# Optimization experiments

Measured on AMD Instinct MI355X. Metric: run time of the kernel, lower is better.

## Reference

```python
import jax, jax.numpy as jnp
import numpy as np

H = 50  # hidden size

def setup_inputs() -> dict:
    key = jax.random.key(0)
    k_in, k_wx, k_wh, k_wd = jax.random.split(key, 4)
    B, T, D = 1024, 2048, 1
    inputs = jax.random.normal(k_in, (B, T, D), dtype=jnp.float32)
    # fused gate weights, gate order (i, f, g, o) -> 4H columns
    Wx = jax.random.normal(k_wx, (D, 4 * H), dtype=jnp.float32) * 0.1
    Wh = jax.random.normal(k_wh, (H, 4 * H), dtype=jnp.float32) * 0.1
    b = jnp.zeros((4 * H,), dtype=jnp.float32)
    Wd = jax.random.normal(k_wd, (H, 1), dtype=jnp.float32) * 0.1
    bd = jnp.zeros((1,), dtype=jnp.float32)
    return {"inputs": inputs, "Wx": Wx, "Wh": Wh, "b": b, "Wd": Wd, "bd": bd}

def _lstm_last_hidden(inputs, Wx, Wh, b):
    B = inputs.shape[0]
    c0 = jnp.zeros((B, H), dtype=inputs.dtype)
    h0 = jnp.zeros((B, H), dtype=inputs.dtype)

    def step(carry, x_t):
        c, h = carry
        z = x_t @ Wx + h @ Wh + b          # [B, 4H]
        i, f, g, o = jnp.split(z, 4, axis=-1)
        i = jax.nn.sigmoid(i)
        f = jax.nn.sigmoid(f)
        g = jnp.tanh(g)
        o = jax.nn.sigmoid(o)
        c_new = f * c + i * g
        h_new = o * jnp.tanh(c_new)
        return (c_new, h_new), None

    xs = jnp.swapaxes(inputs, 0, 1)        # [T, B, D] for scan over time
    (c_fin, h_fin), _ = jax.lax.scan(step, (c0, h0), xs)
    return h_fin                            # [B, H]

def reference(inputs, Wx, Wh, b, Wd, bd):
    h_last = _lstm_last_hidden(inputs, Wx, Wh, b)
    return h_last @ Wd + bd                # [B, 1]
```

## Files before the change

kernel.cpp:

```cpp
#include <hip/hip_runtime.h>

#define HID 50
#define FOURH 200
#define TSTEPS 2048
#define NBATCH 1024

#define LOG2E 1.44269504f

typedef _Float16 v2h __attribute__((ext_vector_type(2)));

__device__ __forceinline__ float frcp(float x)  { return __builtin_amdgcn_rcpf(x); }
__device__ __forceinline__ float fexp2(float x) { return __builtin_amdgcn_exp2f(x); }
__device__ __forceinline__ v2h bc_v2h(unsigned int u) {
    return __builtin_bit_cast(v2h, u);
}

__global__ __launch_bounds__(64, 1)
void lstm_trans_kernel(const float* __restrict__ x,
                       const float* __restrict__ Wx,
                       const float* __restrict__ Wh,
                       const float* __restrict__ bias,
                       const float* __restrict__ Wd,
                       const float* __restrict__ bd,
                       float* __restrict__ out) {
    const int b    = blockIdx.x;
    const int lane = threadIdx.x;
    const int lc   = (lane < HID) ? lane : (HID - 1);

    __shared__ __align__(16) float xs[TSTEPS + 8];

    const float4* xb4 = (const float4*)(x + (size_t)b * TSTEPS);
    float4* xs4 = (float4*)xs;
    #pragma unroll
    for (int i = lane; i < TSTEPS / 4; i += 64) xs4[i] = xb4[i];
    if (lane < 8) xs[TSTEPS + lane] = 0.0f;

    const float SNEG = -LOG2E;
    const float S2L  = 2.0f * LOG2E;
    v2h wi[25], wf[25], wg[25], wo[25];
    #pragma unroll
    for (int k2 = 0; k2 < 25; ++k2) {
        const float* r0 = Wh + (2 * k2) * FOURH;
        const float* r1 = Wh + (2 * k2 + 1) * FOURH;
        wi[k2] = v2h{(_Float16)(SNEG * r0[lc]),           (_Float16)(SNEG * r1[lc])};
        wf[k2] = v2h{(_Float16)(SNEG * r0[HID + lc]),     (_Float16)(SNEG * r1[HID + lc])};
        wg[k2] = v2h{(_Float16)(S2L  * r0[2 * HID + lc]), (_Float16)(S2L  * r1[2 * HID + lc])};
        wo[k2] = v2h{(_Float16)(SNEG * r0[3 * HID + lc]), (_Float16)(SNEG * r1[3 * HID + lc])};
    }
    const float wx_i = SNEG * Wx[lc],           b_i = SNEG * bias[lc];
    const float wx_f = SNEG * Wx[HID + lc],     b_f = SNEG * bias[HID + lc];
    const float wx_g = S2L  * Wx[2 * HID + lc], b_g = S2L  * bias[2 * HID + lc];
    const float wx_o = SNEG * Wx[3 * HID + lc], b_o = SNEG * bias[3 * HID + lc];

    float cs = 0.0f;
    float h  = 0.0f;
    __syncthreads();

    const float4* xsv = (const float4*)xs;
    float4 xq = xsv[0];

    for (int tb = 0; tb < TSTEPS; tb += 4) {
        const float4 xq_next = xsv[(tb >> 2) + 1];

        #pragma unroll
        for (int s = 0; s < 4; ++s) {
            const float xt = (s == 0) ? xq.x : (s == 1) ? xq.y
                           : (s == 2) ? xq.z : xq.w;

            const int hi32 = __builtin_bit_cast(int, h);
            const int hn32 = __builtin_amdgcn_update_dpp(
                0, hi32, 0x101 , 0xf, 0xf, true);
            const float hn = __builtin_bit_cast(float, hn32);
            const unsigned hp =
                __builtin_bit_cast(unsigned, __builtin_amdgcn_cvt_pkrtz(h, hn));
            unsigned sh[25];
            #pragma unroll
            for (int k = 0; k < 25; ++k)
                sh[k] = (unsigned)__builtin_amdgcn_readlane((int)hp, 2 * k);

            float zi = fmaf(xt, wx_i, b_i);
            #pragma unroll
            for (int j = 0; j < 25; ++j)
                zi = __builtin_amdgcn_fdot2(wi[j], bc_v2h(sh[j]), zi, false);
            const float ei = fexp2(zi);

            float zg = fmaf(xt, wx_g, b_g);
            #pragma unroll
            for (int j = 0; j < 25; ++j)
                zg = __builtin_amdgcn_fdot2(wg[j], bc_v2h(sh[j]), zg, false);
            const float eg = fexp2(zg);

            const float den1 = (1.0f + ei) * (1.0f + eg);
            const float r1   = frcp(den1);
            const float num1 = fmaf(eg, S2L, -S2L);
            const float prod = num1 * r1;

            float zf = fmaf(xt, wx_f, b_f);
            #pragma unroll
            for (int j = 0; j < 25; ++j)
                zf = __builtin_amdgcn_fdot2(wf[j], bc_v2h(sh[j]), zf, false);
            const float ef = fexp2(zf);
            const float fg = frcp(1.0f + ef);

            const float cs_new = fmaf(fg, cs, prod);
            const float ec = fexp2(cs_new);

            float zo = fmaf(xt, wx_o, b_o);
            #pragma unroll
            for (int j = 0; j < 25; ++j)
                zo = __builtin_amdgcn_fdot2(wo[j], bc_v2h(sh[j]), zo, false);
            const float eo = fexp2(zo);

            const float den2 = (1.0f + eo) * (1.0f + ec);
            const float r2   = frcp(den2);
            const float num2 = ec - 1.0f;
            cs = cs_new;
            h  = num2 * r2;
        }

        xq = xq_next;
    }

    float v = (lane < HID) ? h * Wd[lane] : 0.0f;
    #pragma unroll
    for (int off = 32; off > 0; off >>= 1) v += __shfl_down(v, off);
    if (lane == 0) out[b] = v + bd[0];
}

extern "C" void kernel_launch(void* const* d_in, const int* in_sizes, int n_in,
                              void* d_out, int out_size, void* d_ws, size_t ws_size,
                              hipStream_t stream) {
    const float* x    = (const float*)d_in[0];
    const float* Wx   = (const float*)d_in[1];
    const float* Wh   = (const float*)d_in[2];
    const float* bias = (const float*)d_in[3];
    const float* Wd   = (const float*)d_in[4];
    const float* bd   = (const float*)d_in[5];
    float* out = (float*)d_out;

    lstm_trans_kernel<<<dim3(NBATCH), dim3(64), 0, stream>>>(
        x, Wx, Wh, bias, Wd, bd, out);
}
```

Before: 642.7 us.

## Broadcast half of hidden state via LDS, fuse gate dot loops and reciprocals

Splits the per-step broadcast of the hidden state: the first 24 elements still go through readlane, and the remaining 26 are written as fp16 to a small LDS buffer and read back as vector loads. This cuts the number of scalar readlane instructions on the serial recurrence path. It also interleaves the i/g/f dot-product chains for more instruction-level parallelism and merges the forget-gate reciprocal into a single rcp. The LDS write-then-read within one wave has no explicit barrier and depends on in-order LDS access within the wave. The added LDS round trip sits on the recurrence's critical latency path.

```diff
diff --git a/kernel.cpp b/kernel.cpp
--- a/kernel.cpp
+++ b/kernel.cpp
@@ -16,24 +16,26 @@
 }
 
 __global__ __launch_bounds__(64, 1)
-void lstm_trans_kernel(const float* __restrict__ x,
-                       const float* __restrict__ Wx,
-                       const float* __restrict__ Wh,
-                       const float* __restrict__ bias,
-                       const float* __restrict__ Wd,
-                       const float* __restrict__ bd,
-                       float* __restrict__ out) {
+void lstm_hyb_kernel(const float* __restrict__ x,
+                     const float* __restrict__ Wx,
+                     const float* __restrict__ Wh,
+                     const float* __restrict__ bias,
+                     const float* __restrict__ Wd,
+                     const float* __restrict__ bd,
+                     float* __restrict__ out) {
     const int b    = blockIdx.x;
     const int lane = threadIdx.x;
     const int lc   = (lane < HID) ? lane : (HID - 1);
 
-    __shared__ __align__(16) float xs[TSTEPS + 8];
+    __shared__ __align__(16) float    xs[TSTEPS + 8];
+    __shared__ __align__(16) _Float16 hbuf[80];
 
     const float4* xb4 = (const float4*)(x + (size_t)b * TSTEPS);
     float4* xs4 = (float4*)xs;
     #pragma unroll
     for (int i = lane; i < TSTEPS / 4; i += 64) xs4[i] = xb4[i];
     if (lane < 8) xs[TSTEPS + lane] = 0.0f;
+    for (int i = lane; i < 80; i += 64) hbuf[i] = (_Float16)0.0f;
 
     const float SNEG = -LOG2E;
     const float S2L  = 2.0f * LOG2E;
@@ -52,6 +54,8 @@
     const float wx_g = S2L  * Wx[2 * HID + lc], b_g = S2L  * bias[2 * HID + lc];
     const float wx_o = SNEG * Wx[3 * HID + lc], b_o = SNEG * bias[3 * HID + lc];
 
+    const int widx = (lane < HID) ? lane : (lane + 14);
+
     float cs = 0.0f;
     float h  = 0.0f;
     __syncthreads();
@@ -67,55 +71,76 @@
             const float xt = (s == 0) ? xq.x : (s == 1) ? xq.y
                            : (s == 2) ? xq.z : xq.w;
 
+            const uint4    q0  = *(const uint4*)(hbuf + 24);
+            const uint4    q1  = *(const uint4*)(hbuf + 32);
+            const uint4    q2  = *(const uint4*)(hbuf + 40);
+            const unsigned q3  = *(const unsigned*)(hbuf + 48);
+            const unsigned hl[13] = {q0.x, q0.y, q0.z, q0.w,
+                                     q1.x, q1.y, q1.z, q1.w,
+                                     q2.x, q2.y, q2.z, q2.w, q3};
+
             const int hi32 = __builtin_bit_cast(int, h);
             const int hn32 = __builtin_amdgcn_update_dpp(
                 0, hi32, 0x101 , 0xf, 0xf, true);
             const float hn = __builtin_bit_cast(float, hn32);
             const unsigned hp =
                 __builtin_bit_cast(unsigned, __builtin_amdgcn_cvt_pkrtz(h, hn));
-            unsigned sh[25];
+            unsigned sh[12];
             #pragma unroll
-            for (int k = 0; k < 25; ++k)
+            for (int k = 0; k < 12; ++k)
                 sh[k] = (unsigned)__builtin_amdgcn_readlane((int)hp, 2 * k);
 
             float zi = fmaf(xt, wx_i, b_i);
-            #pragma unroll
-            for (int j = 0; j < 25; ++j)
-                zi = __builtin_amdgcn_fdot2(wi[j], bc_v2h(sh[j]), zi, false);
-            const float ei = fexp2(zi);
-
             float zg = fmaf(xt, wx_g, b_g);
-            #pragma unroll
-            for (int j = 0; j < 25; ++j)
-                zg = __builtin_amdgcn_fdot2(wg[j], bc_v2h(sh[j]), zg, false);
-            const float eg = fexp2(zg);
-
-            const float den1 = (1.0f + ei) * (1.0f + eg);
-            const float r1   = frcp(den1);
-            const float num1 = fmaf(eg, S2L, -S2L);
-            const float prod = num1 * r1;
-
             float zf = fmaf(xt, wx_f, b_f);
             #pragma unroll
-            for (int j = 0; j < 25; ++j)
-                zf = __builtin_amdgcn_fdot2(wf[j], bc_v2h(sh[j]), zf, false);
+            for (int j = 0; j < 12; ++j) {
+                const v2h hj = bc_v2h(sh[j]);
+                zi = __builtin_amdgcn_fdot2(wi[j], hj, zi, false);
+                zg = __builtin_amdgcn_fdot2(wg[j], hj, zg, false);
+                zf = __builtin_amdgcn_fdot2(wf[j], hj, zf, false);
+            }
+            #pragma unroll
+            for (int j = 0; j < 13; ++j) {
+                const v2h hj = bc_v2h(hl[j]);
+                zi = __builtin_amdgcn_fdot2(wi[12 + j], hj, zi, false);
+                zg = __builtin_amdgcn_fdot2(wg[12 + j], hj, zg, false);
+                zf = __builtin_amdgcn_fdot2(wf[12 + j], hj, zf, false);
+            }
+            const float ei = fexp2(zi);
+            const float eg = fexp2(zg);
             const float ef = fexp2(zf);
-            const float fg = frcp(1.0f + ef);
 
-            const float cs_new = fmaf(fg, cs, prod);
+            const float a1   = 1.0f + ei;
+            const float a2   = 1.0f + eg;
+            const float den1 = a1 * a2;
+            const float num1 = fmaf(eg, S2L, -S2L);
+            const float a3   = 1.0f + ef;
+            const float dd   = den1 * a3;
+            const float rr   = frcp(dd);
+            const float m1   = num1 * a3;
+            const float tnum = fmaf(cs, den1, m1);
+            const float cs_new = tnum * rr;
             const float ec = fexp2(cs_new);
 
             float zo = fmaf(xt, wx_o, b_o);
             #pragma unroll
-            for (int j = 0; j < 25; ++j)
+            for (int j = 0; j < 12; ++j)
                 zo = __builtin_amdgcn_fdot2(wo[j], bc_v2h(sh[j]), zo, false);
+            #pragma unroll
+            for (int j = 0; j < 13; ++j)
+                zo = __builtin_amdgcn_fdot2(wo[12 + j], bc_v2h(hl[j]), zo, false);
             const float eo = fexp2(zo);
 
-            const float den2 = (1.0f + eo) * (1.0f + ec);
+            const float a4   = 1.0f + eo;
+            const float a5   = 1.0f + ec;
+            const float den2 = a4 * a5;
             const float r2   = frcp(den2);
             const float num2 = ec - 1.0f;
             cs = cs_new;
             h  = num2 * r2;
+
+            hbuf[widx] = (_Float16)h;
         }
 
         xq = xq_next;
@@ -138,6 +163,6 @@
     const float* bd   = (const float*)d_in[5];
     float* out = (float*)d_out;
 
-    lstm_trans_kernel<<<dim3(NBATCH), dim3(64), 0, stream>>>(
+    lstm_hyb_kernel<<<dim3(NBATCH), dim3(64), 0, stream>>>(
         x, Wx, Wh, bias, Wd, bd, out);
 }
```

Result: no change. 648.2 us (+0.9%).

## Interleave gate dot chains, merge reciprocals, and shorten neighbour-hidden exchange path

Applied to the files above, without the earlier changes.

Runs the i, g and f gate dot-product chains interleaved in one loop so the dependent fdot2 sequences can overlap. The cell update now uses a single reciprocal over the product of the three denominators instead of two. The DPP neighbour shuffle is applied to the numerator and reciprocal as soon as they exist, and hn is rebuilt by a multiply, which moves the exchange off the h-to-readlane critical path. The bias/input affine terms use packed float2 arithmetic. Combining three denominators into one product may lose range or precision.

```diff
diff --git a/kernel.cpp b/kernel.cpp
--- a/kernel.cpp
+++ b/kernel.cpp
@@ -8,6 +8,7 @@
 #define LOG2E 1.44269504f
 
 typedef _Float16 v2h __attribute__((ext_vector_type(2)));
+typedef float    f32x2 __attribute__((ext_vector_type(2)));
 
 __device__ __forceinline__ float frcp(float x)  { return __builtin_amdgcn_rcpf(x); }
 __device__ __forceinline__ float fexp2(float x) { return __builtin_amdgcn_exp2f(x); }
@@ -16,13 +17,13 @@
 }
 
 __global__ __launch_bounds__(64, 1)
-void lstm_trans_kernel(const float* __restrict__ x,
-                       const float* __restrict__ Wx,
-                       const float* __restrict__ Wh,
-                       const float* __restrict__ bias,
-                       const float* __restrict__ Wd,
-                       const float* __restrict__ bd,
-                       float* __restrict__ out) {
+void lstm_pk_kernel(const float* __restrict__ x,
+                    const float* __restrict__ Wx,
+                    const float* __restrict__ Wh,
+                    const float* __restrict__ bias,
+                    const float* __restrict__ Wd,
+                    const float* __restrict__ bd,
+                    float* __restrict__ out) {
     const int b    = blockIdx.x;
     const int lane = threadIdx.x;
     const int lc   = (lane < HID) ? lane : (HID - 1);
@@ -47,13 +48,14 @@
         wg[k2] = v2h{(_Float16)(S2L  * r0[2 * HID + lc]), (_Float16)(S2L  * r1[2 * HID + lc])};
         wo[k2] = v2h{(_Float16)(SNEG * r0[3 * HID + lc]), (_Float16)(SNEG * r1[3 * HID + lc])};
     }
-    const float wx_i = SNEG * Wx[lc],           b_i = SNEG * bias[lc];
-    const float wx_f = SNEG * Wx[HID + lc],     b_f = SNEG * bias[HID + lc];
-    const float wx_g = S2L  * Wx[2 * HID + lc], b_g = S2L  * bias[2 * HID + lc];
-    const float wx_o = SNEG * Wx[3 * HID + lc], b_o = SNEG * bias[3 * HID + lc];
+    const f32x2 wx_if = {SNEG * Wx[lc],           SNEG * Wx[HID + lc]};
+    const f32x2 b_if  = {SNEG * bias[lc],         SNEG * bias[HID + lc]};
+    const f32x2 wx_go = {S2L  * Wx[2 * HID + lc], SNEG * Wx[3 * HID + lc]};
+    const f32x2 b_go  = {S2L  * bias[2 * HID + lc], SNEG * bias[3 * HID + lc]};
 
     float cs = 0.0f;
     float h  = 0.0f;
+    float hn = 0.0f;
     __syncthreads();
 
     const float4* xsv = (const float4*)xs;
@@ -67,10 +69,6 @@
             const float xt = (s == 0) ? xq.x : (s == 1) ? xq.y
                            : (s == 2) ? xq.z : xq.w;
 
-            const int hi32 = __builtin_bit_cast(int, h);
-            const int hn32 = __builtin_amdgcn_update_dpp(
-                0, hi32, 0x101 , 0xf, 0xf, true);
-            const float hn = __builtin_bit_cast(float, hn32);
             const unsigned hp =
                 __builtin_bit_cast(unsigned, __builtin_amdgcn_cvt_pkrtz(h, hn));
             unsigned sh[25];
@@ -78,44 +76,53 @@
             for (int k = 0; k < 25; ++k)
                 sh[k] = (unsigned)__builtin_amdgcn_readlane((int)hp, 2 * k);
 
-            float zi = fmaf(xt, wx_i, b_i);
+            const f32x2 xt2 = {xt, xt};
+            const f32x2 zif0 = xt2 * wx_if + b_if;
+            const f32x2 zgo0 = xt2 * wx_go + b_go;
+            float zi = zif0.x, zf = zif0.y, zg = zgo0.x, zo = zgo0.y;
+
+            #pragma unroll
+            for (int j = 0; j < 25; ++j) {
+                const v2h hj = bc_v2h(sh[j]);
+                zi = __builtin_amdgcn_fdot2(wi[j], hj, zi, false);
+                zg = __builtin_amdgcn_fdot2(wg[j], hj, zg, false);
+                zf = __builtin_amdgcn_fdot2(wf[j], hj, zf, false);
+            }
+            const float ei = fexp2(zi);
+            const float eg = fexp2(zg);
+            const float ef = fexp2(zf);
+
+            const f32x2 eig = {ei, eg};
+            const f32x2 a12 = eig + f32x2{1.0f, 1.0f};
+            const float den1 = a12.x * a12.y;
+            const float num1 = fmaf(eg, S2L, -S2L);
+            const float a3   = 1.0f + ef;
+            const float dd   = den1 * a3;
+            const float rr   = frcp(dd);
+            const float m1   = num1 * a3;
+            const float tnum = fmaf(cs, den1, m1);
+            const float cs_new = tnum * rr;
+            const float ec = fexp2(cs_new);
+
+            float zov = zo;
             #pragma unroll
             for (int j = 0; j < 25; ++j)
-                zi = __builtin_amdgcn_fdot2(wi[j], bc_v2h(sh[j]), zi, false);
-            const float ei = fexp2(zi);
+                zov = __builtin_amdgcn_fdot2(wo[j], bc_v2h(sh[j]), zov, false);
+            const float eo = fexp2(zov);
 
-            float zg = fmaf(xt, wx_g, b_g);
-            #pragma unroll
-            for (int j = 0; j < 25; ++j)
-                zg = __builtin_amdgcn_fdot2(wg[j], bc_v2h(sh[j]), zg, false);
-            const float eg = fexp2(zg);
-
-            const float den1 = (1.0f + ei) * (1.0f + eg);
-            const float r1   = frcp(den1);
-            const float num1 = fmaf(eg, S2L, -S2L);
-            const float prod = num1 * r1;
-
-            float zf = fmaf(xt, wx_f, b_f);
-            #pragma unroll
-            for (int j = 0; j < 25; ++j)
-                zf = __builtin_amdgcn_fdot2(wf[j], bc_v2h(sh[j]), zf, false);
-            const float ef = fexp2(zf);
-            const float fg = frcp(1.0f + ef);
-
-            const float cs_new = fmaf(fg, cs, prod);
-            const float ec = fexp2(cs_new);
-
-            float zo = fmaf(xt, wx_o, b_o);
-            #pragma unroll
-            for (int j = 0; j < 25; ++j)
-                zo = __builtin_amdgcn_fdot2(wo[j], bc_v2h(sh[j]), zo, false);
-            const float eo = fexp2(zo);
-
-            const float den2 = (1.0f + eo) * (1.0f + ec);
+            const f32x2 eoc = {eo, ec};
+            const f32x2 a45 = eoc + f32x2{1.0f, 1.0f};
+            const float den2 = a45.x * a45.y;
             const float r2   = frcp(den2);
             const float num2 = ec - 1.0f;
             cs = cs_new;
             h  = num2 * r2;
+
+            const int n2 = __builtin_amdgcn_update_dpp(
+                0, __builtin_bit_cast(int, num2), 0x101, 0xf, 0xf, true);
+            const int r2n = __builtin_amdgcn_update_dpp(
+                0, __builtin_bit_cast(int, r2), 0x101, 0xf, 0xf, true);
+            hn = __builtin_bit_cast(float, n2) * __builtin_bit_cast(float, r2n);
         }
 
         xq = xq_next;
@@ -138,6 +145,6 @@
     const float* bd   = (const float*)d_in[5];
     float* out = (float*)d_out;
 
-    lstm_trans_kernel<<<dim3(NBATCH), dim3(64), 0, stream>>>(
+    lstm_pk_kernel<<<dim3(NBATCH), dim3(64), 0, stream>>>(
         x, Wx, Wh, bias, Wd, bd, out);
 }
```

New measurement: 644.8 us. No clear change (+0.3%).
